# Performance work log

Hardware: AMD Instinct MI355X
Metric: run time of the kernel (lower is better)

Reference implementation:

```python
import jax, jax.numpy as jnp
import numpy as np

TAU = 0.08


def setup_inputs() -> dict:
    key = jax.random.key(0)
    k1, k2 = jax.random.split(key)
    pos_waves = jax.random.normal(k1, (32, 64, 8192), dtype=jnp.float32)
    neg_waves = jax.random.normal(k2, (32, 64, 8192), dtype=jnp.float32)
    return {"pos_waves": pos_waves, "neg_waves": neg_waves}


def _normalize(w):
    # global min/max over the whole wave tensor (matches torch.min/torch.max on 2D tensor)
    lo = jnp.min(w, axis=(1, 2), keepdims=True)  # [N,1,1]
    hi = jnp.max(w, axis=(1, 2), keepdims=True)
    return (w - lo) / (hi - lo)


def _pairwise_negpearson(X, Y):
    # X: [N,B,T], Y: [M,B,T] -> mean over B of (1 - pearson) for every (n,m) pair
    T = X.shape[-1]
    sx = jnp.sum(X, axis=-1)            # [N,B]
    sy = jnp.sum(Y, axis=-1)            # [M,B]
    sx2 = jnp.sum(X * X, axis=-1)       # [N,B]
    sy2 = jnp.sum(Y * Y, axis=-1)       # [M,B]
    sxy = jnp.einsum('nbt,mbt->nmb', X, Y)  # [N,M,B]
    num = T * sxy - sx[:, None, :] * sy[None, :, :]
    den = jnp.sqrt((T * sx2 - sx * sx)[:, None, :] * (T * sy2 - sy * sy)[None, :, :])
    return jnp.mean(1.0 - num / den, axis=-1)  # [N,M]


def reference(pos_waves, neg_waves):
    P = _normalize(pos_waves)   # [N,B,T]
    Q = _normalize(neg_waves)   # [M,B,T]
    N = P.shape[0]

    d_pp = _pairwise_negpearson(P, P)                    # [N,N]
    upper = jnp.triu(jnp.ones((N, N), dtype=bool), k=1)  # i < j pairs only
    pos_total = jnp.sum(jnp.where(upper, jnp.exp(d_pp / TAU), 0.0))

    d_pn = _pairwise_negpearson(P, Q)                    # [N,M]
    neg_total = jnp.sum(jnp.exp(d_pn / TAU))

    return jnp.log10(pos_total / neg_total + 1.0)
```

## Files before the change

kernel.cpp:

```cpp
#include <hip/hip_runtime.h>
#include <cmath>

#define N_ 32
#define B_ 64
#define T_ 8192
#define NBLK1 1024
#define PS 2176

typedef _Float16 half4 __attribute__((ext_vector_type(4)));
typedef _Float16 half8 __attribute__((ext_vector_type(8)));
typedef float floatx4 __attribute__((ext_vector_type(4)));

__global__ __launch_bounds__(512, 4)
void k_stage1(const float* __restrict__ pos, const float* __restrict__ neg,
              float* __restrict__ partial, double* __restrict__ accs,
              unsigned* __restrict__ ctr) {
    __shared__ __align__(16) _Float16 tile[2][32][512];
    const int bid = blockIdx.x;
    const int b = bid & 63, cg = bid >> 6;
    const int tid = threadIdx.x;
    const int w = tid >> 6, lane = tid & 63;
    const int m = lane & 15, h = lane >> 4;

    if (bid == 0 && tid == 0) { accs[0] = 0.0; accs[1] = 0.0; *ctr = 0u; }

    float* out = partial + (long)bid * PS;
    const long cbase = (long)cg * 512;

    float4 v[16];
#pragma unroll
    for (int s = 0; s < 4; ++s) {
        const float4* prow = (const float4*)(pos + ((long)(4 * w + s) * B_ + b) * T_ + cbase);
        v[s * 2 + 0] = prow[lane];
        v[s * 2 + 1] = prow[64 + lane];
    }
#pragma unroll
    for (int s = 0; s < 4; ++s) {
        const float4* nrow = (const float4*)(neg + ((long)(4 * w + s) * B_ + b) * T_ + cbase);
        v[8 + s * 2 + 0] = nrow[lane];
        v[8 + s * 2 + 1] = nrow[64 + lane];
    }

    float st[16];
#pragma unroll
    for (int i = 0; i < 16; ++i) st[i] = 0.f;

#pragma unroll
    for (int t2 = 0; t2 < 2; ++t2) {
#pragma unroll
        for (int s = 0; s < 4; ++s) {
            const int r = 4 * w + s;
            const int xr = (r & 7) << 4;
#pragma unroll
            for (int j = 0; j < 2; ++j) {
                float4 q = v[t2 * 8 + s * 2 + j];
                st[t2 * 8 + s * 2 + 0] += q.x + q.y + q.z + q.w;
                float sq = st[t2 * 8 + s * 2 + 1];
                sq = fmaf(q.x, q.x, sq); sq = fmaf(q.y, q.y, sq);
                sq = fmaf(q.z, q.z, sq); sq = fmaf(q.w, q.w, sq);
                st[t2 * 8 + s * 2 + 1] = sq;
                half4 hq = {(_Float16)q.x, (_Float16)q.y, (_Float16)q.z, (_Float16)q.w};
                char* dst = (char*)&tile[t2][r][0] + ((j * 512 + lane * 8) ^ xr);
                *(half4*)dst = hq;
            }
        }
    }

#pragma unroll
    for (int i = 0; i < 16; ++i) {
        float x = st[i];
        x += __shfl_xor(x, 1);  x += __shfl_xor(x, 2);  x += __shfl_xor(x, 4);
        x += __shfl_xor(x, 8);  x += __shfl_xor(x, 16); x += __shfl_xor(x, 32);
        st[i] = x;
    }
    if (lane == 0) {
#pragma unroll
        for (int t2 = 0; t2 < 2; ++t2)
#pragma unroll
            for (int s = 0; s < 4; ++s) {
                out[2048 + t2 * 64 + (4 * w + s)]      = st[t2 * 8 + s * 2 + 0];
                out[2048 + t2 * 64 + 32 + (4 * w + s)] = st[t2 * 8 + s * 2 + 1];
            }
    }

    __syncthreads();

    const int mat = w >> 2, qi = (w >> 1) & 1, qj = w & 1;
    const int arow = qi * 16 + m, brow = qj * 16 + m;
    const char* tA = (const char*)&tile[0][arow][0];
    const char* tB = (const char*)&tile[mat][brow][0];
    const int xa = (arow & 7) << 4, xb = (brow & 7) << 4;

    floatx4 acc = {};
#pragma unroll
    for (int kk = 0; kk < 16; ++kk) {
        half8 af = *(const half8*)(tA + ((kk * 64 + h * 16) ^ xa));
        half8 bf = *(const half8*)(tB + ((kk * 64 + h * 16) ^ xb));
        acc = __builtin_amdgcn_mfma_f32_16x16x32_f16(af, bf, acc, 0, 0, 0);
    }

#pragma unroll
    for (int reg = 0; reg < 4; ++reg) {
        const int rr = qi * 16 + h * 4 + reg;
        const int cc = qj * 16 + m;
        out[mat * 1024 + rr * 32 + cc] = acc[reg];
    }
}

__global__ void k_reduce(const float* __restrict__ partial, float* __restrict__ red) {
    const int b = blockIdx.y;
    const int o = blockIdx.x * 128 + threadIdx.x;
    float s = 0.f;
#pragma unroll
    for (int c = 0; c < 16; ++c) s += partial[(long)(c * 64 + b) * PS + o];
    red[(long)b * PS + o] = s;
}

__global__ __launch_bounds__(256)
void k_entries(const float* __restrict__ red, double* __restrict__ accs,
               unsigned* __restrict__ ctr, float* __restrict__ out) {
    const int tid = threadIdx.x;
    const int w = tid >> 6, lane = tid & 63;
    const int entry = blockIdx.x * 4 + w;
    const int mat = entry >> 10;
    const int idx = entry & 1023;
    const int n = idx >> 5, m = idx & 31;

    const float* rb = red + (long)lane * PS;
    const float g    = rb[mat * 1024 + idx];
    const float sxn  = rb[2048 + n];
    const float sx2n = rb[2080 + n];
    const float sym  = rb[mat ? 2112 + m : 2048 + m];
    const float sy2m = rb[mat ? 2144 + m : 2080 + m];

    double num = (double)T_ * (double)g - (double)sxn * (double)sym;
    double vx = (double)T_ * (double)sx2n - (double)sxn * (double)sxn;
    double vy = (double)T_ * (double)sy2m - (double)sym * (double)sym;
    double contrib = 1.0 - num / sqrt(vx * vy);

#pragma unroll
    for (int off = 32; off; off >>= 1) contrib += __shfl_down(contrib, off);

    __shared__ double s_pos[4], s_neg[4];
    if (lane == 0) {
        double d = contrib * (1.0 / B_);
        double term = exp(d / 0.08);
        double p = 0.0, q = 0.0;
        if (mat == 0) { if (n < m) p = term; }
        else q = term;
        s_pos[w] = p; s_neg[w] = q;
    }
    __syncthreads();
    if (tid == 0) {
        atomicAdd(&accs[0], s_pos[0] + s_pos[1] + s_pos[2] + s_pos[3]);
        atomicAdd(&accs[1], s_neg[0] + s_neg[1] + s_neg[2] + s_neg[3]);
        __threadfence();
        const unsigned old = atomicAdd(ctr, 1u);
        if (old == gridDim.x - 1) {
            __threadfence();
            const double p = ((volatile double*)accs)[0];
            const double q = ((volatile double*)accs)[1];
            out[0] = (float)log10(p / q + 1.0);
        }
    }
}

extern "C" void kernel_launch(void* const* d_in, const int* in_sizes, int n_in,
                              void* d_out, int out_size, void* d_ws, size_t ws_size,
                              hipStream_t stream) {
    (void)in_sizes; (void)n_in; (void)out_size; (void)ws_size;
    const float* pos = (const float*)d_in[0];
    const float* neg = (const float*)d_in[1];
    float* out = (float*)d_out;

    char* ws = (char*)d_ws;
    float* partial = (float*)ws;
    float* red = (float*)(ws + (size_t)NBLK1 * PS * 4);
    double* accs = (double*)(ws + (size_t)NBLK1 * PS * 4 + (size_t)64 * PS * 4);
    unsigned* ctr = (unsigned*)((char*)accs + 16);

    k_stage1<<<NBLK1, 512, 0, stream>>>(pos, neg, partial, accs, ctr);
    k_reduce<<<dim3(17, 64), 128, 0, stream>>>(partial, red);
    k_entries<<<512, 256, 0, stream>>>(red, accs, ctr, out);
}
```

Measured before the change: 173.5 us.

## Stream stage-1 inputs straight to LDS with global_load_lds in two chunks

```diff
diff --git a/kernel.cpp b/kernel.cpp
--- a/kernel.cpp
+++ b/kernel.cpp
@@ -7,103 +7,99 @@
 #define NBLK1 1024
 #define PS 2176
 
-typedef _Float16 half4 __attribute__((ext_vector_type(4)));
 typedef _Float16 half8 __attribute__((ext_vector_type(8)));
 typedef float floatx4 __attribute__((ext_vector_type(4)));
+
+__device__ __forceinline__ void gload16(const float* g, void* lds) {
+    __builtin_amdgcn_global_load_lds(
+        (const __attribute__((address_space(1))) void*)g,
+        (__attribute__((address_space(3))) void*)lds, 16, 0, 0);
+}
 
 __global__ __launch_bounds__(512, 4)
 void k_stage1(const float* __restrict__ pos, const float* __restrict__ neg,
               float* __restrict__ partial, double* __restrict__ accs,
               unsigned* __restrict__ ctr) {
-    __shared__ __align__(16) _Float16 tile[2][32][512];
+    __shared__ __align__(16) float tile[2][32][256];
     const int bid = blockIdx.x;
     const int b = bid & 63, cg = bid >> 6;
     const int tid = threadIdx.x;
     const int w = tid >> 6, lane = tid & 63;
     const int m = lane & 15, h = lane >> 4;
+    const int mat = w >> 2, qi = (w >> 1) & 1, qj = w & 1;
+    const int arow = qi * 16 + m, brow = qj * 16 + m;
 
     if (bid == 0 && tid == 0) { accs[0] = 0.0; accs[1] = 0.0; *ctr = 0u; }
 
-    float* out = partial + (long)bid * PS;
-    const long cbase = (long)cg * 512;
+    floatx4 acc = {};
+    float s1[8], s2[8];
+#pragma unroll
+    for (int j = 0; j < 8; ++j) { s1[j] = 0.f; s2[j] = 0.f; }
 
-    float4 v[16];
+    const long tb0 = (long)cg * 512;
+
 #pragma unroll
-    for (int s = 0; s < 4; ++s) {
-        const float4* prow = (const float4*)(pos + ((long)(4 * w + s) * B_ + b) * T_ + cbase);
-        v[s * 2 + 0] = prow[lane];
-        v[s * 2 + 1] = prow[64 + lane];
-    }
+    for (int ck = 0; ck < 2; ++ck) {
 #pragma unroll
-    for (int s = 0; s < 4; ++s) {
-        const float4* nrow = (const float4*)(neg + ((long)(4 * w + s) * B_ + b) * T_ + cbase);
-        v[8 + s * 2 + 0] = nrow[lane];
-        v[8 + s * 2 + 1] = nrow[64 + lane];
+        for (int i = 0; i < 8; ++i) {
+            const int lin = w * 8 + i;
+            const int r = lin & 31;
+            const float* base = (lin & 32) ? neg : pos;
+            const float* src = base + ((long)r * B_ + b) * T_ + tb0 + ck * 256 + lane * 4;
+            gload16(src, (char*)tile + (long)lin * 1024);
+        }
+        __syncthreads();
+
+#pragma unroll
+        for (int j = 0; j < 8; ++j) {
+            const float4* rp = (const float4*)((char*)tile + (long)(w * 8 + j) * 1024);
+            float4 q = rp[lane];
+            s1[j] += q.x + q.y + q.z + q.w;
+            s2[j] = fmaf(q.x, q.x, s2[j]); s2[j] = fmaf(q.y, q.y, s2[j]);
+            s2[j] = fmaf(q.z, q.z, s2[j]); s2[j] = fmaf(q.w, q.w, s2[j]);
+        }
+
+#pragma unroll
+        for (int kk = 0; kk < 8; ++kk) {
+            const float* ta = &tile[0][arow][kk * 32 + h * 8];
+            const float* tb = &tile[mat][brow][kk * 32 + h * 8];
+            float4 a0 = *(const float4*)ta, a1 = *(const float4*)(ta + 4);
+            float4 b0 = *(const float4*)tb, b1 = *(const float4*)(tb + 4);
+            half8 af = {(_Float16)a0.x, (_Float16)a0.y, (_Float16)a0.z, (_Float16)a0.w,
+                        (_Float16)a1.x, (_Float16)a1.y, (_Float16)a1.z, (_Float16)a1.w};
+            half8 bf = {(_Float16)b0.x, (_Float16)b0.y, (_Float16)b0.z, (_Float16)b0.w,
+                        (_Float16)b1.x, (_Float16)b1.y, (_Float16)b1.z, (_Float16)b1.w};
+            acc = __builtin_amdgcn_mfma_f32_16x16x32_f16(af, bf, acc, 0, 0, 0);
+        }
+        __syncthreads();
     }
 
-    float st[16];
-#pragma unroll
-    for (int i = 0; i < 16; ++i) st[i] = 0.f;
-
-#pragma unroll
-    for (int t2 = 0; t2 < 2; ++t2) {
-#pragma unroll
-        for (int s = 0; s < 4; ++s) {
-            const int r = 4 * w + s;
-            const int xr = (r & 7) << 4;
-#pragma unroll
-            for (int j = 0; j < 2; ++j) {
-                float4 q = v[t2 * 8 + s * 2 + j];
-                st[t2 * 8 + s * 2 + 0] += q.x + q.y + q.z + q.w;
-                float sq = st[t2 * 8 + s * 2 + 1];
-                sq = fmaf(q.x, q.x, sq); sq = fmaf(q.y, q.y, sq);
-                sq = fmaf(q.z, q.z, sq); sq = fmaf(q.w, q.w, sq);
-                st[t2 * 8 + s * 2 + 1] = sq;
-                half4 hq = {(_Float16)q.x, (_Float16)q.y, (_Float16)q.z, (_Float16)q.w};
-                char* dst = (char*)&tile[t2][r][0] + ((j * 512 + lane * 8) ^ xr);
-                *(half4*)dst = hq;
-            }
-        }
-    }
-
-#pragma unroll
-    for (int i = 0; i < 16; ++i) {
-        float x = st[i];
-        x += __shfl_xor(x, 1);  x += __shfl_xor(x, 2);  x += __shfl_xor(x, 4);
-        x += __shfl_xor(x, 8);  x += __shfl_xor(x, 16); x += __shfl_xor(x, 32);
-        st[i] = x;
-    }
-    if (lane == 0) {
-#pragma unroll
-        for (int t2 = 0; t2 < 2; ++t2)
-#pragma unroll
-            for (int s = 0; s < 4; ++s) {
-                out[2048 + t2 * 64 + (4 * w + s)]      = st[t2 * 8 + s * 2 + 0];
-                out[2048 + t2 * 64 + 32 + (4 * w + s)] = st[t2 * 8 + s * 2 + 1];
-            }
-    }
-
-    __syncthreads();
-
-    const int mat = w >> 2, qi = (w >> 1) & 1, qj = w & 1;
-    const int arow = qi * 16 + m, brow = qj * 16 + m;
-    const char* tA = (const char*)&tile[0][arow][0];
-    const char* tB = (const char*)&tile[mat][brow][0];
-    const int xa = (arow & 7) << 4, xb = (brow & 7) << 4;
-
-    floatx4 acc = {};
-#pragma unroll
-    for (int kk = 0; kk < 16; ++kk) {
-        half8 af = *(const half8*)(tA + ((kk * 64 + h * 16) ^ xa));
-        half8 bf = *(const half8*)(tB + ((kk * 64 + h * 16) ^ xb));
-        acc = __builtin_amdgcn_mfma_f32_16x16x32_f16(af, bf, acc, 0, 0, 0);
-    }
+    float* out = partial + (long)bid * PS;
 
 #pragma unroll
     for (int reg = 0; reg < 4; ++reg) {
         const int rr = qi * 16 + h * 4 + reg;
         const int cc = qj * 16 + m;
         out[mat * 1024 + rr * 32 + cc] = acc[reg];
+    }
+
+#pragma unroll
+    for (int j = 0; j < 8; ++j) {
+        s1[j] += __shfl_xor(s1[j], 1);  s1[j] += __shfl_xor(s1[j], 2);
+        s1[j] += __shfl_xor(s1[j], 4);  s1[j] += __shfl_xor(s1[j], 8);
+        s1[j] += __shfl_xor(s1[j], 16); s1[j] += __shfl_xor(s1[j], 32);
+        s2[j] += __shfl_xor(s2[j], 1);  s2[j] += __shfl_xor(s2[j], 2);
+        s2[j] += __shfl_xor(s2[j], 4);  s2[j] += __shfl_xor(s2[j], 8);
+        s2[j] += __shfl_xor(s2[j], 16); s2[j] += __shfl_xor(s2[j], 32);
+    }
+    float v1 = s1[0], v2 = s2[0];
+#pragma unroll
+    for (int j = 1; j < 8; ++j)
+        if (lane == j) { v1 = s1[j]; v2 = s2[j]; }
+    if (lane < 8) {
+        const int tr = w * 8 + lane;
+        out[2048 + (tr >> 5) * 64 + (tr & 31)] = v1;
+        out[2048 + (tr >> 5) * 64 + 32 + (tr & 31)] = v2;
     }
 }
 
```

Measured after the change: 242.4 us. +39.7%, slower.
